# Kernel optimization log

Measured on AMD Instinct MI355X. Metric: run time of the kernel, lower is better.

The kernel has to match this reference:

```python
import jax, jax.numpy as jnp
import numpy as np

L = 16384   # nodes (rows)
E = 131072  # edges
SP = 20000  # column positions (nodes + periodic images)
C = 512     # embed_dim
H = 8       # heads
DH = C // H # head dim = 64
HID = 1024  # ffn hidden


def setup_inputs() -> dict:
    key = jax.random.key(0)
    ks = jax.random.split(key, 16)
    p = lambda k, shape: jax.random.normal(k, shape, dtype=jnp.float32) * 0.02
    return dict(
        x=jax.random.normal(ks[0], (L, C), dtype=jnp.float32),
        row_index=jax.random.randint(ks[1], (E,), 0, L),
        col_index=jax.random.randint(ks[2], (E,), 0, L),
        to_col_index=jax.random.randint(ks[3], (E,), 0, SP),
        att_bias=jax.random.normal(ks[4], (E, H), dtype=jnp.float32),
        pos_att_bias=jax.random.normal(ks[5], (E, H), dtype=jnp.float32),
        dist=jax.random.uniform(ks[6], (E,), minval=0.5, maxval=5.0),
        pos=jax.random.normal(ks[7], (L, 3), dtype=jnp.float32),
        col_pos=jax.random.normal(ks[8], (SP, 3), dtype=jnp.float32),
        ln1_g=jnp.ones((C,), jnp.float32), ln1_b=jnp.zeros((C,), jnp.float32),
        ln2_g=jnp.ones((C,), jnp.float32), ln2_b=jnp.zeros((C,), jnp.float32),
        Wq=p(ks[9], (C, C)), bq=jnp.zeros((C,), jnp.float32),
        Wk=p(ks[10], (C, C)), bk=jnp.zeros((C,), jnp.float32),
        Wv=p(ks[11], (C, C)), bv=jnp.zeros((C,), jnp.float32),
        Wvec=p(ks[12], (3, C)), bvec=jnp.zeros((C,), jnp.float32),
        Wo=p(ks[13], (C, C)), bo=jnp.zeros((C,), jnp.float32),
        W1=p(ks[14], (C, HID)), b1=jnp.zeros((HID,), jnp.float32),
        W2=p(ks[15], (HID, C)), b2=jnp.zeros((C,), jnp.float32),
    )


def _ln(x, g, b, eps=1e-5):
    mu = jnp.mean(x, -1, keepdims=True)
    v = jnp.mean((x - mu) ** 2, -1, keepdims=True)
    return (x - mu) * jax.lax.rsqrt(v + eps) * g + b


def reference(x, row_index, col_index, to_col_index, att_bias, pos_att_bias,
              dist, pos, col_pos, ln1_g, ln1_b, ln2_g, ln2_b,
              Wq, bq, Wk, bk, Wv, bv, Wvec, bvec, Wo, bo, W1, b1, W2, b2):
    Lx = x.shape[0]
    # --- pre-norm + Euclidean sparse attention ---
    z = _ln(x, ln1_g, ln1_b)
    q = (z @ Wq + bq).reshape(Lx, H, DH)
    k = (z @ Wk + bk).reshape(Lx, H, DH)
    v = (z @ Wv + bv).reshape(Lx, H, DH)
    qe = q[row_index]          # (E,H,DH) gather
    ke = k[col_index]          # (E,H,DH)
    ve = v[col_index]          # (E,H,DH)
    # relative unit direction from receiving node to (PBC-shifted) column node
    rel = (col_pos[to_col_index] - pos[row_index]) / dist[:, None]   # (E,3)
    ve = ve + (rel @ Wvec + bvec).reshape(-1, H, DH)
    # Euclidean (negative squared L2) attention score + positional bias
    score = -jnp.sum((qe - ke) ** 2, axis=-1) / np.float32(np.sqrt(DH)) + pos_att_bias  # (E,H)
    # segment softmax over edges grouped by row_index
    m = jax.ops.segment_max(score, row_index, num_segments=Lx)       # (L,H)
    m = jnp.where(jnp.isfinite(m), m, 0.0)
    pexp = jnp.exp(score - m[row_index])
    den = jax.ops.segment_sum(pexp, row_index, num_segments=Lx)      # (L,H)
    deng = den[row_index]
    alpha = pexp / jnp.where(deng == 0.0, 1.0, deng)                 # (E,H)
    out = jax.ops.segment_sum(alpha[:, :, None] * ve, row_index, num_segments=Lx)
    att = out.reshape(Lx, C) @ Wo + bo
    x = x + att
    # --- pre-norm + feed-forward ---
    z2 = _ln(x, ln2_g, ln2_b)
    ff = jax.nn.gelu(z2 @ W1 + b1) @ W2 + b2
    return x + ff
```

## Files before the change

### kernel.cpp

```cpp
#include <hip/hip_runtime.h>

#define L_NODES 16384
#define E_EDGES 131072
#define CDIM 512
#define QKVDIM 1536
#define HEADS 8
#define DHEAD 64
#define HID 1024

typedef __attribute__((ext_vector_type(8))) short bf16x8;
typedef __attribute__((ext_vector_type(4))) float f32x4;

__device__ inline unsigned short f2b(float f) {
    union { float f; unsigned int u; } v{f};
    unsigned int r = (v.u + 0x7fffu + ((v.u >> 16) & 1u)) >> 16;
    return (unsigned short)r;
}
__device__ inline float b2f(unsigned short h) {
    union { unsigned int u; float f; } v;
    v.u = (unsigned int)h << 16;
    return v.f;
}

__device__ inline void async_lds16(const void* g, void* l) {
    __builtin_amdgcn_global_load_lds(
        (const __attribute__((address_space(1))) unsigned int*)g,
        (__attribute__((address_space(3))) unsigned int*)l,
        16, 0, 0);
}

__global__ __launch_bounds__(256) void ln_bf16_kernel(
    const float* __restrict__ x, const float* __restrict__ g,
    const float* __restrict__ b, short* __restrict__ out)
{
    int row = blockIdx.x;
    int t = threadIdx.x;
    const float2* xr = (const float2*)(x + (size_t)row * CDIM);
    float2 v = xr[t];
    float s = v.x + v.y;
    float sq = v.x * v.x + v.y * v.y;
    for (int off = 32; off; off >>= 1) {
        s += __shfl_xor(s, off);
        sq += __shfl_xor(sq, off);
    }
    __shared__ float ss[4], sqs[4];
    int wave = t >> 6, lane = t & 63;
    if (lane == 0) { ss[wave] = s; sqs[wave] = sq; }
    __syncthreads();
    s = ss[0] + ss[1] + ss[2] + ss[3];
    sq = sqs[0] + sqs[1] + sqs[2] + sqs[3];
    float mu = s * (1.0f / CDIM);
    float var = sq * (1.0f / CDIM) - mu * mu;
    float inv = rsqrtf(var + 1e-5f);
    int c = t * 2;
    unsigned short h0 = f2b((v.x - mu) * inv * g[c] + b[c]);
    unsigned short h1 = f2b((v.y - mu) * inv * g[c + 1] + b[c + 1]);
    unsigned int packed = ((unsigned int)h1 << 16) | h0;
    *(unsigned int*)(out + (size_t)row * CDIM + c) = packed;
}

__global__ __launch_bounds__(256) void prep_kernel(
    const float* __restrict__ Wq, const float* __restrict__ Wk,
    const float* __restrict__ Wv, const float* __restrict__ Wo,
    const float* __restrict__ W1, const float* __restrict__ W2,
    short* __restrict__ wqkvT, short* __restrict__ woT,
    short* __restrict__ w1T, short* __restrict__ w2T,
    const float* __restrict__ bq, const float* __restrict__ bk,
    const float* __restrict__ bv, float* __restrict__ bqkv,
    int* __restrict__ cnt)
{
    int bid = blockIdx.x;
    if (bid >= 2054) {
        cnt[(bid - 2054) * 256 + threadIdx.x] = 0;
        return;
    }
    if (bid >= 2048) {
        int i = (bid - 2048) * 256 + threadIdx.x;
        float val = (i < CDIM) ? bq[i] : (i < 2 * CDIM) ? bk[i - CDIM] : bv[i - 2 * CDIM];
        bqkv[i] = val;
        return;
    }
    const float* W; short* WT; int K, N, tn, tk;
    if (bid < 1024) {
        int w = bid >> 8, local = bid & 255;
        tn = local & 15; tk = local >> 4; K = 512; N = 512;
        W = (w == 0) ? Wq : (w == 1) ? Wk : (w == 2) ? Wv : Wo;
        WT = (w == 3) ? woT : wqkvT + (size_t)w * 512 * 512;
    } else if (bid < 1536) {
        int local = bid - 1024;
        tn = local & 31; tk = local >> 5; K = 512; N = 1024;
        W = W1; WT = w1T;
    } else {
        int local = bid - 1536;
        tn = local & 15; tk = local >> 4; K = 1024; N = 512;
        W = W2; WT = w2T;
    }
    __shared__ float tile[32][33];
    int tx = threadIdx.x & 31, ty = threadIdx.x >> 5;
    int n0 = tn * 32, k0 = tk * 32;
#pragma unroll
    for (int r = 0; r < 4; r++)
        tile[ty + r * 8][tx] = W[(size_t)(k0 + ty + r * 8) * N + n0 + tx];
    __syncthreads();
#pragma unroll
    for (int r = 0; r < 4; r++)
        WT[(size_t)(n0 + ty + r * 8) * K + k0 + tx] = f2b(tile[tx][ty + r * 8]);
}

__global__ __launch_bounds__(256) void gemm_bf16_kernel(
    const short* __restrict__ A, const short* __restrict__ B,
    const float* __restrict__ bias, const float* __restrict__ res,
    float* __restrict__ outf, short* __restrict__ outb,
    int M, int N, int K, int act)
{
    __shared__ short As[2][128 * 32];
    __shared__ short Bs[2][128 * 32];
    int t = threadIdx.x;
    int bm = blockIdx.y * 128, bn = blockIdx.x * 128;
    int wave = t >> 6, lane = t & 63;
    int wm = (wave & 1) * 64, wn = (wave >> 1) * 64;
    int crow = lane & 15, quad = lane >> 4;

    f32x4 acc[4][4] = {};

    const int niter = K >> 5;
#pragma unroll
    for (int c = 0; c < 2; c++) {
        int idx = c * 256 + t;
        int row = idx >> 2, chunk = idx & 3;
        async_lds16(A + (size_t)(bm + row) * K + chunk * 8,
                    (char*)As + c * 4096 + wave * 1024 + lane * 16);
        async_lds16(B + (size_t)(bn + row) * K + chunk * 8,
                    (char*)Bs + c * 4096 + wave * 1024 + lane * 16);
    }

    for (int i = 0; i < niter; ++i) {
        int cur = i & 1;
        asm volatile("s_waitcnt vmcnt(0)" ::: "memory");
        __builtin_amdgcn_s_barrier();
        if (i + 1 < niter) {
            int k0 = (i + 1) << 5;
            int nxt = cur ^ 1;
#pragma unroll
            for (int c = 0; c < 2; c++) {
                int idx = c * 256 + t;
                int row = idx >> 2, chunk = idx & 3;
                async_lds16(A + (size_t)(bm + row) * K + k0 + chunk * 8,
                            (char*)As + nxt * 8192 + c * 4096 + wave * 1024 + lane * 16);
                async_lds16(B + (size_t)(bn + row) * K + k0 + chunk * 8,
                            (char*)Bs + nxt * 8192 + c * 4096 + wave * 1024 + lane * 16);
            }
        }
        const short* Ab = (const short*)((const char*)As + cur * 8192);
        const short* Bb = (const short*)((const char*)Bs + cur * 8192);
        bf16x8 af[4], bg[4];
#pragma unroll
        for (int ii = 0; ii < 4; ii++)
            af[ii] = *(const bf16x8*)&Ab[(wm + ii * 16 + crow) * 32 + quad * 8];
#pragma unroll
        for (int j = 0; j < 4; j++)
            bg[j] = *(const bf16x8*)&Bb[(wn + j * 16 + crow) * 32 + quad * 8];
#pragma unroll
        for (int ii = 0; ii < 4; ii++)
#pragma unroll
            for (int j = 0; j < 4; j++)
                acc[ii][j] = __builtin_amdgcn_mfma_f32_16x16x32_bf16(af[ii], bg[j], acc[ii][j], 0, 0, 0);
    }

#pragma unroll
    for (int i = 0; i < 4; i++) {
#pragma unroll
        for (int j = 0; j < 4; j++) {
            int n = bn + wn + j * 16 + crow;
            float bi = bias ? bias[n] : 0.0f;
#pragma unroll
            for (int r = 0; r < 4; r++) {
                int mrow = bm + wm + i * 16 + quad * 4 + r;
                float val = acc[i][j][r] + bi;
                if (act) {
                    float u = 1.5957691216057308f * (val + 0.044715f * val * val * val);
                    val = val / (1.0f + __expf(-u));
                }
                if (res) val += res[(size_t)mrow * N + n];
                if (outf) outf[(size_t)mrow * N + n] = val;
                if (outb) outb[(size_t)mrow * N + n] = f2b(val);
            }
        }
    }
}

__global__ void hist_kernel(const int* __restrict__ row_index, int* __restrict__ cnt)
{
    int e = blockIdx.x * 256 + threadIdx.x;
    if (e < E_EDGES) atomicAdd(&cnt[row_index[e]], 1);
}

__global__ void scan_kernel(const int* __restrict__ cnt, int* __restrict__ row_start,
                            int* __restrict__ cursor)
{
    int t = threadIdx.x;
    const int PER = L_NODES / 64;
    int local = 0;
    for (int i = 0; i < PER; i++) local += cnt[t * PER + i];
    int v = local;
    for (int off = 1; off < 64; off <<= 1) {
        int u = __shfl_up(v, off);
        if (t >= off) v += u;
    }
    int run = v - local;
    for (int i = 0; i < PER; i++) {
        row_start[t * PER + i] = run;
        cursor[t * PER + i] = run;
        run += cnt[t * PER + i];
    }
    if (t == 63) row_start[L_NODES] = run;
}

__global__ void scatter_kernel(const int* __restrict__ row_index, const int* __restrict__ col_index,
                               const int* __restrict__ to_col_index, const float* __restrict__ dist,
                               const float* __restrict__ pos, const float* __restrict__ col_pos,
                               const float* __restrict__ pos_att_bias,
                               int* __restrict__ cursor, int4* __restrict__ emeta,
                               float* __restrict__ pabp)
{
    int e = blockIdx.x * 256 + threadIdx.x;
    if (e < E_EDGES) {
        int row = row_index[e];
        int p = atomicAdd(&cursor[row], 1);
        int tci = to_col_index[e];
        float dinv = 1.0f / dist[e];
        float r0 = (col_pos[tci * 3]     - pos[row * 3])     * dinv;
        float r1 = (col_pos[tci * 3 + 1] - pos[row * 3 + 1]) * dinv;
        float r2 = (col_pos[tci * 3 + 2] - pos[row * 3 + 2]) * dinv;
        emeta[p] = make_int4(col_index[e], __float_as_int(r0), __float_as_int(r1),
                             __float_as_int(r2));
        const float4* pb = (const float4*)(pos_att_bias + (size_t)e * HEADS);
        float4 b0 = pb[0], b1 = pb[1];
        float4* dst = (float4*)(pabp + (size_t)p * HEADS);
        dst[0] = b0; dst[1] = b1;
    }
}

__global__ __launch_bounds__(256) void attn_kernel(
    const short* __restrict__ qkv, const int4* __restrict__ emeta,
    const float* __restrict__ pabp, const int* __restrict__ row_start,
    const float* __restrict__ Wvec, const float* __restrict__ bvec,
    short* __restrict__ out_bf)
{
    int lane = threadIdx.x & 63;
    int r = blockIdx.x * 4 + (threadIdx.x >> 6);
    int h = lane >> 3;
    int cbase = lane * 8;

    float qv[8], wv0[8], wv1[8], wv2[8], bvv[8];
    {
        bf16x8 qh = *(const bf16x8*)(qkv + (size_t)r * QKVDIM + cbase);
#pragma unroll
        for (int j = 0; j < 8; j++) qv[j] = b2f((unsigned short)qh[j]);
        float4 a0 = *(const float4*)(Wvec + cbase);
        float4 a1 = *(const float4*)(Wvec + cbase + 4);
        float4 b0 = *(const float4*)(Wvec + CDIM + cbase);
        float4 b1 = *(const float4*)(Wvec + CDIM + cbase + 4);
        float4 c0 = *(const float4*)(Wvec + 2 * CDIM + cbase);
        float4 c1 = *(const float4*)(Wvec + 2 * CDIM + cbase + 4);
        float4 d0 = *(const float4*)(bvec + cbase);
        float4 d1 = *(const float4*)(bvec + cbase + 4);
        wv0[0]=a0.x; wv0[1]=a0.y; wv0[2]=a0.z; wv0[3]=a0.w; wv0[4]=a1.x; wv0[5]=a1.y; wv0[6]=a1.z; wv0[7]=a1.w;
        wv1[0]=b0.x; wv1[1]=b0.y; wv1[2]=b0.z; wv1[3]=b0.w; wv1[4]=b1.x; wv1[5]=b1.y; wv1[6]=b1.z; wv1[7]=b1.w;
        wv2[0]=c0.x; wv2[1]=c0.y; wv2[2]=c0.z; wv2[3]=c0.w; wv2[4]=c1.x; wv2[5]=c1.y; wv2[6]=c1.z; wv2[7]=c1.w;
        bvv[0]=d0.x; bvv[1]=d0.y; bvv[2]=d0.z; bvv[3]=d0.w; bvv[4]=d1.x; bvv[5]=d1.y; bvv[6]=d1.z; bvv[7]=d1.w;
    }

    int e0 = row_start[r], e1 = row_start[r + 1];
    float m = -1e30f, l = 0.0f;
    float acc[8] = {};

    int4 em_n, em_n2;
    float pab_n;
    bf16x8 k_n, v_n;
    if (e0 < e1) {
        em_n = emeta[e0];
        em_n2 = emeta[(e0 + 1 < e1) ? e0 + 1 : e1 - 1];
        pab_n = pabp[(size_t)e0 * HEADS + h];
        const short* kp = qkv + (size_t)em_n.x * QKVDIM + CDIM + cbase;
        k_n = *(const bf16x8*)kp;
        v_n = *(const bf16x8*)(kp + CDIM);
    }
    for (int idx = e0; idx < e1; ++idx) {
        int4 em = em_n;
        float pab = pab_n;
        bf16x8 k8 = k_n, v8 = v_n;
        em_n = em_n2;
        int i2 = (idx + 2 < e1) ? idx + 2 : e1 - 1;
        em_n2 = emeta[i2];
        int i1 = (idx + 1 < e1) ? idx + 1 : e1 - 1;
        pab_n = pabp[(size_t)i1 * HEADS + h];
        {
            const short* kp = qkv + (size_t)em_n.x * QKVDIM + CDIM + cbase;
            k_n = *(const bf16x8*)kp;
            v_n = *(const bf16x8*)(kp + CDIM);
        }
        float s = 0.0f;
        float vf[8];
#pragma unroll
        for (int j = 0; j < 8; j++) {
            float kf = b2f((unsigned short)k8[j]);
            vf[j] = b2f((unsigned short)v8[j]);
            float d = qv[j] - kf;
            s = fmaf(d, d, s);
        }
        s += __shfl_xor(s, 1);
        s += __shfl_xor(s, 2);
        s += __shfl_xor(s, 4);
        float score = -s * 0.125f + pab;
        float mn = fmaxf(m, score);
        float scale = __expf(m - mn);
        float pexp = __expf(score - mn);
        m = mn;
        l = l * scale + pexp;
        float r0 = __int_as_float(em.y), r1 = __int_as_float(em.z), r2 = __int_as_float(em.w);
#pragma unroll
        for (int j = 0; j < 8; j++) {
            float vv = vf[j] + r0 * wv0[j] + r1 * wv1[j] + r2 * wv2[j] + bvv[j];
            acc[j] = fmaf(acc[j], scale, pexp * vv);
        }
    }
    float inv = (l > 0.0f) ? 1.0f / l : 0.0f;
    bf16x8 o;
#pragma unroll
    for (int j = 0; j < 8; j++) o[j] = (short)f2b(acc[j] * inv);
    *(bf16x8*)(out_bf + (size_t)r * CDIM + cbase) = o;
}

extern "C" void kernel_launch(void* const* d_in, const int* in_sizes, int n_in,
                              void* d_out, int out_size, void* d_ws, size_t ws_size,
                              hipStream_t stream)
{
    const float* x            = (const float*)d_in[0];
    const int*   row_index    = (const int*)d_in[1];
    const int*   col_index    = (const int*)d_in[2];
    const int*   to_col_index = (const int*)d_in[3];
    const float* pos_att_bias = (const float*)d_in[5];
    const float* dist         = (const float*)d_in[6];
    const float* pos          = (const float*)d_in[7];
    const float* col_pos      = (const float*)d_in[8];
    const float* ln1_g = (const float*)d_in[9];
    const float* ln1_b = (const float*)d_in[10];
    const float* ln2_g = (const float*)d_in[11];
    const float* ln2_b = (const float*)d_in[12];
    const float* Wq = (const float*)d_in[13];  const float* bq = (const float*)d_in[14];
    const float* Wk = (const float*)d_in[15];  const float* bk = (const float*)d_in[16];
    const float* Wv = (const float*)d_in[17];  const float* bv = (const float*)d_in[18];
    const float* Wvec = (const float*)d_in[19]; const float* bvec = (const float*)d_in[20];
    const float* Wo = (const float*)d_in[21];  const float* bo = (const float*)d_in[22];
    const float* W1 = (const float*)d_in[23];  const float* b1 = (const float*)d_in[24];
    const float* W2 = (const float*)d_in[25];  const float* b2 = (const float*)d_in[26];

    char* ws = (char*)d_ws;
    size_t off = 0;
    auto alloc = [&](size_t bytes) -> void* {
        void* p = ws + off;
        off = (off + bytes + 255) & ~(size_t)255;
        return p;
    };
    const size_t LC = (size_t)L_NODES * CDIM;
    short* qkvb = (short*)alloc((size_t)L_NODES * QKVDIM * 2);
    float* x1f  = (float*)alloc(LC * 4);
    short* zbf  = (short*)alloc(LC * 2);
    short* abf  = (short*)alloc(LC * 2);
    short* wqkvT = (short*)alloc((size_t)QKVDIM * CDIM * 2);
    short* woT   = (short*)alloc((size_t)CDIM * CDIM * 2);
    short* w1T   = (short*)alloc((size_t)CDIM * HID * 2);
    short* w2T   = (short*)alloc((size_t)HID * CDIM * 2);
    float* bqkv  = (float*)alloc(QKVDIM * 4);
    int* cnt       = (int*)alloc(L_NODES * 4);
    int* cursor    = (int*)alloc(L_NODES * 4);
    int* row_start = (int*)alloc((L_NODES + 1) * 4);
    int4* emeta    = (int4*)alloc((size_t)E_EDGES * 16);
    short* hbf = (short*)qkvb;
    float* pabp = x1f;

    prep_kernel<<<2118, 256, 0, stream>>>(Wq, Wk, Wv, Wo, W1, W2,
                                          wqkvT, woT, w1T, w2T,
                                          bq, bk, bv, bqkv, cnt);

    ln_bf16_kernel<<<L_NODES, 256, 0, stream>>>(x, ln1_g, ln1_b, zbf);

    dim3 gqkv(QKVDIM / 128, L_NODES / 128);
    gemm_bf16_kernel<<<gqkv, 256, 0, stream>>>(zbf, wqkvT, bqkv, nullptr, nullptr, qkvb,
                                               L_NODES, QKVDIM, CDIM, 0);

    hist_kernel<<<E_EDGES / 256, 256, 0, stream>>>(row_index, cnt);
    scan_kernel<<<1, 64, 0, stream>>>(cnt, row_start, cursor);
    scatter_kernel<<<E_EDGES / 256, 256, 0, stream>>>(row_index, col_index, to_col_index,
                                                      dist, pos, col_pos, pos_att_bias,
                                                      cursor, emeta, pabp);

    attn_kernel<<<L_NODES / 4, 256, 0, stream>>>(qkvb, emeta, pabp, row_start, Wvec, bvec, abf);

    dim3 g512(CDIM / 128, L_NODES / 128);
    gemm_bf16_kernel<<<g512, 256, 0, stream>>>(abf, woT, bo, x, x1f, nullptr, L_NODES, CDIM, CDIM, 0);

    ln_bf16_kernel<<<L_NODES, 256, 0, stream>>>(x1f, ln2_g, ln2_b, zbf);

    dim3 g1024(HID / 128, L_NODES / 128);
    gemm_bf16_kernel<<<g1024, 256, 0, stream>>>(zbf, w1T, b1, nullptr, nullptr, hbf, L_NODES, HID, CDIM, 1);
    gemm_bf16_kernel<<<g512, 256, 0, stream>>>(hbf, w2T, b2, x1f, (float*)d_out, nullptr, L_NODES, CDIM, HID, 0);
}
```

Baseline: 427.4 us.

## Triple-buffer GEMM LDS pipeline and use 64-row tiles for N=512 GEMMs

The bf16 GEMM moves from a double-buffered to a triple-buffered LDS pipeline. Loads are issued two k-steps ahead, and a partial vmcnt wait lets the next stage's loads stay in flight during compute. The kernel is templated on the M tile size, and the Wo and W2 GEMMs (N=512) use BM=64 to double their block count and improve occupancy across CUs. The cost is more LDS per block and fewer MFMAs per fragment load for the smaller tiles.

```diff
diff --git a/kernel.cpp b/kernel.cpp
--- a/kernel.cpp
+++ b/kernel.cpp
@@ -107,68 +107,77 @@
         WT[(size_t)(n0 + ty + r * 8) * K + k0 + tx] = f2b(tile[tx][ty + r * 8]);
 }
 
+template<int BM>
 __global__ __launch_bounds__(256) void gemm_bf16_kernel(
     const short* __restrict__ A, const short* __restrict__ B,
     const float* __restrict__ bias, const float* __restrict__ res,
     float* __restrict__ outf, short* __restrict__ outb,
     int M, int N, int K, int act)
 {
-    __shared__ short As[2][128 * 32];
-    __shared__ short Bs[2][128 * 32];
+    constexpr int MI = BM / 32;
+    constexpr int LPI_A = BM / 64;
+    constexpr int STAGE_A = BM * 64;
+    constexpr int STAGE_B = 8192;
+    __shared__ short As[3 * BM * 32];
+    __shared__ short Bs[3 * 128 * 32];
     int t = threadIdx.x;
-    int bm = blockIdx.y * 128, bn = blockIdx.x * 128;
+    int bm = blockIdx.y * BM, bn = blockIdx.x * 128;
     int wave = t >> 6, lane = t & 63;
-    int wm = (wave & 1) * 64, wn = (wave >> 1) * 64;
+    int wm = (wave & 1) * (BM / 2), wn = (wave >> 1) * 64;
     int crow = lane & 15, quad = lane >> 4;
 
-    f32x4 acc[4][4] = {};
+    f32x4 acc[MI][4] = {};
 
     const int niter = K >> 5;
-#pragma unroll
-    for (int c = 0; c < 2; c++) {
-        int idx = c * 256 + t;
-        int row = idx >> 2, chunk = idx & 3;
-        async_lds16(A + (size_t)(bm + row) * K + chunk * 8,
-                    (char*)As + c * 4096 + wave * 1024 + lane * 16);
-        async_lds16(B + (size_t)(bn + row) * K + chunk * 8,
-                    (char*)Bs + c * 4096 + wave * 1024 + lane * 16);
-    }
+    auto stage = [&](int s, int k0) {
+#pragma unroll
+        for (int a = 0; a < LPI_A; a++) {
+            int idx = a * 256 + t;
+            int row = idx >> 2, chunk = idx & 3;
+            async_lds16(A + (size_t)(bm + row) * K + k0 + chunk * 8,
+                        (char*)As + s * STAGE_A + idx * 16);
+        }
+#pragma unroll
+        for (int c = 0; c < 2; c++) {
+            int idx = c * 256 + t;
+            int row = idx >> 2, chunk = idx & 3;
+            async_lds16(B + (size_t)(bn + row) * K + k0 + chunk * 8,
+                        (char*)Bs + s * STAGE_B + idx * 16);
+        }
+    };
+
+    stage(0, 0);
+    stage(1, 32);
 
     for (int i = 0; i < niter; ++i) {
-        int cur = i & 1;
-        asm volatile("s_waitcnt vmcnt(0)" ::: "memory");
+        int cur = i % 3;
+        if (i + 1 < niter) {
+            if constexpr (BM == 128) asm volatile("s_waitcnt vmcnt(4)" ::: "memory");
+            else                     asm volatile("s_waitcnt vmcnt(3)" ::: "memory");
+        } else {
+            asm volatile("s_waitcnt vmcnt(0)" ::: "memory");
+        }
         __builtin_amdgcn_s_barrier();
-        if (i + 1 < niter) {
-            int k0 = (i + 1) << 5;
-            int nxt = cur ^ 1;
-#pragma unroll
-            for (int c = 0; c < 2; c++) {
-                int idx = c * 256 + t;
-                int row = idx >> 2, chunk = idx & 3;
-                async_lds16(A + (size_t)(bm + row) * K + k0 + chunk * 8,
-                            (char*)As + nxt * 8192 + c * 4096 + wave * 1024 + lane * 16);
-                async_lds16(B + (size_t)(bn + row) * K + k0 + chunk * 8,
-                            (char*)Bs + nxt * 8192 + c * 4096 + wave * 1024 + lane * 16);
-            }
-        }
-        const short* Ab = (const short*)((const char*)As + cur * 8192);
-        const short* Bb = (const short*)((const char*)Bs + cur * 8192);
-        bf16x8 af[4], bg[4];
-#pragma unroll
-        for (int ii = 0; ii < 4; ii++)
+        if (i + 2 < niter) stage((i + 2) % 3, (i + 2) << 5);
+
+        const short* Ab = As + cur * (BM * 32);
+        const short* Bb = Bs + cur * (128 * 32);
+        bf16x8 af[MI], bg[4];
+#pragma unroll
+        for (int ii = 0; ii < MI; ii++)
             af[ii] = *(const bf16x8*)&Ab[(wm + ii * 16 + crow) * 32 + quad * 8];
 #pragma unroll
         for (int j = 0; j < 4; j++)
             bg[j] = *(const bf16x8*)&Bb[(wn + j * 16 + crow) * 32 + quad * 8];
 #pragma unroll
-        for (int ii = 0; ii < 4; ii++)
+        for (int ii = 0; ii < MI; ii++)
 #pragma unroll
             for (int j = 0; j < 4; j++)
                 acc[ii][j] = __builtin_amdgcn_mfma_f32_16x16x32_bf16(af[ii], bg[j], acc[ii][j], 0, 0, 0);
     }
 
 #pragma unroll
-    for (int i = 0; i < 4; i++) {
+    for (int i = 0; i < MI; i++) {
 #pragma unroll
         for (int j = 0; j < 4; j++) {
             int n = bn + wn + j * 16 + crow;
@@ -387,8 +396,8 @@
     ln_bf16_kernel<<<L_NODES, 256, 0, stream>>>(x, ln1_g, ln1_b, zbf);
 
     dim3 gqkv(QKVDIM / 128, L_NODES / 128);
-    gemm_bf16_kernel<<<gqkv, 256, 0, stream>>>(zbf, wqkvT, bqkv, nullptr, nullptr, qkvb,
-                                               L_NODES, QKVDIM, CDIM, 0);
+    gemm_bf16_kernel<128><<<gqkv, 256, 0, stream>>>(zbf, wqkvT, bqkv, nullptr, nullptr, qkvb,
+                                                    L_NODES, QKVDIM, CDIM, 0);
 
     hist_kernel<<<E_EDGES / 256, 256, 0, stream>>>(row_index, cnt);
     scan_kernel<<<1, 64, 0, stream>>>(cnt, row_start, cursor);
@@ -398,12 +407,13 @@
 
     attn_kernel<<<L_NODES / 4, 256, 0, stream>>>(qkvb, emeta, pabp, row_start, Wvec, bvec, abf);
 
-    dim3 g512(CDIM / 128, L_NODES / 128);
-    gemm_bf16_kernel<<<g512, 256, 0, stream>>>(abf, woT, bo, x, x1f, nullptr, L_NODES, CDIM, CDIM, 0);
+    dim3 gwo(CDIM / 128, L_NODES / 64);
+    gemm_bf16_kernel<64><<<gwo, 256, 0, stream>>>(abf, woT, bo, x, x1f, nullptr, L_NODES, CDIM, CDIM, 0);
 
     ln_bf16_kernel<<<L_NODES, 256, 0, stream>>>(x1f, ln2_g, ln2_b, zbf);
 
     dim3 g1024(HID / 128, L_NODES / 128);
-    gemm_bf16_kernel<<<g1024, 256, 0, stream>>>(zbf, w1T, b1, nullptr, nullptr, hbf, L_NODES, HID, CDIM, 1);
-    gemm_bf16_kernel<<<g512, 256, 0, stream>>>(hbf, w2T, b2, x1f, (float*)d_out, nullptr, L_NODES, CDIM, HID, 0);
-}
+    gemm_bf16_kernel<128><<<g1024, 256, 0, stream>>>(zbf, w1T, b1, nullptr, nullptr, hbf, L_NODES, HID, CDIM, 1);
+    dim3 gw2(CDIM / 128, L_NODES / 64);
+    gemm_bf16_kernel<64><<<gw2, 256, 0, stream>>>(hbf, w2T, b2, x1f, (float*)d_out, nullptr, L_NODES, CDIM, HID, 0);
+}
```

After: 411.6 us. 3.7% less time.
